# Kernel tuning notes

Hardware: AMD Instinct MI355X
Metric: run time of the kernel (lower is better)

Reference implementation:

```python
import jax, jax.numpy as jnp
import numpy as np

TEMPERATURE = 0.07
BASE_TEMPERATURE = 0.07
EPS = 1e-12


def setup_inputs() -> dict:
    key = jax.random.key(0)
    features = jax.random.normal(key, (4096, 2, 128), dtype=jnp.float32)
    return {"features": features}


def reference(features):
    bsz, n_views, d = features.shape
    n = bsz * n_views
    # torch.cat(torch.unbind(features, dim=1), dim=0): view-major stacking -> [N, D]
    cf = jnp.swapaxes(features, 0, 1).reshape(n, d)
    # L2-normalize rows
    cf = cf / jnp.linalg.norm(cf, axis=-1, keepdims=True)
    # Pairwise L2 distance via Gram matrix: ||a-b||^2 = 2 - 2 a.b for unit vectors.
    # Equivalent math to (cf[:,None]-cf).norm(dim=-1) without the (N,N,D) intermediate.
    gram = cf @ cf.T  # [N, N]
    dist = jnp.sqrt(jnp.clip(2.0 - 2.0 * gram, EPS))
    anchor_dot_contrast = 1.0 - dist  # [N, N]
    logits_max = jax.lax.stop_gradient(jnp.max(anchor_dot_contrast, axis=1, keepdims=True))
    logits = anchor_dot_contrast - logits_max
    # positives mask: same original sample, different row/col in tiled layout
    mask = jnp.tile(jnp.eye(bsz, dtype=jnp.float32), (n_views, n_views))  # [N, N]
    logits_mask = 1.0 - jnp.eye(n, dtype=jnp.float32)  # exclude self
    mask = mask * logits_mask
    exp_logits = jnp.exp(logits) * logits_mask
    log_prob = logits - jnp.log(jnp.sum(exp_logits, axis=1, keepdims=True))
    mean_log_prob_pos = jnp.sum(mask * log_prob, axis=1) / jnp.sum(mask, axis=1)
    loss = -(TEMPERATURE / BASE_TEMPERATURE) * mean_log_prob_pos
    return jnp.mean(loss.reshape(n_views, bsz))
```

## Files before the change

### kernel.cpp

```cpp
#include <hip/hip_runtime.h>
#include <math.h>

#define BSZ   4096
#define NROWS 8192
#define DIM   128
#define EPSC  1e-12f

#define JS  8
#define NJT 8

typedef _Float16 half8 __attribute__((ext_vector_type(8)));
typedef float    f32x4 __attribute__((ext_vector_type(4)));

typedef __attribute__((address_space(1))) const unsigned int gas_u32;
typedef __attribute__((address_space(3))) unsigned int       las_u32;

__device__ __forceinline__ void stageB(_Float16* lds, const char* gsrc, int w, int lane) {
    #pragma unroll
    for (int it = 0; it < 8; ++it) {
        int c = w * 8 + it;
        __builtin_amdgcn_global_load_lds(
            (gas_u32*)(gsrc + c * 1024 + lane * 16),
            (las_u32*)((char*)lds + c * 1024), 16, 0, 0);
    }
}

__global__ __launch_bounds__(256) void norm_zero_kernel(
    const float* __restrict__ feat, float* __restrict__ cf,
    unsigned int* __restrict__ hsw, float* __restrict__ s, float* __restrict__ out)
{
    int t = blockIdx.x * 256 + threadIdx.x;
    if (t < NROWS) s[t] = 0.0f;
    if (t == 0) out[0] = 0.0f;

    int row  = t >> 6;
    int lane = t & 63;
    int v = row >> 12;
    int b = row & 4095;
    const float* src = feat + (size_t)b * 256 + (size_t)v * 128;
    float2 x = *(const float2*)(src + lane * 2);
    float ss = x.x * x.x + x.y * x.y;
    #pragma unroll
    for (int m = 32; m >= 1; m >>= 1) ss += __shfl_xor(ss, m, 64);
    float inv = 1.0f / sqrtf(ss);
    float2 o; o.x = x.x * inv; o.y = x.y * inv;
    *(float2*)(cf + (size_t)row * DIM + lane * 2) = o;

    union { _Float16 h[2]; unsigned int u; } cv;
    cv.h[0] = (_Float16)o.x;
    cv.h[1] = (_Float16)o.y;
    size_t off = (size_t)row * 256 + ((lane * 4) ^ ((row & 7) << 4));
    *(unsigned int*)((char*)hsw + off) = cv.u;
}

__global__ __launch_bounds__(256, 2) void gram_kernel(
    const _Float16* __restrict__ h, float* __restrict__ s)
{
    __shared__ _Float16 bbuf[2][128 * 128];

    int t    = threadIdx.x;
    int w    = t >> 6;
    int lane = t & 63;
    int r16  = lane & 15;
    int g    = lane >> 4;
    int wr   = w >> 1, wc = w & 1;
    int rb   = blockIdx.x >> 3;
    int js   = blockIdx.x & (JS - 1);
    int i0   = rb * 128;
    int rowbase = wr * 64;
    int swz  = (r16 & 7) << 4;
    const char* hb = (const char*)h;

    half8 A[4][4];
    #pragma unroll
    for (int f = 0; f < 4; ++f) {
        size_t rowoff = (size_t)(i0 + rowbase + f * 16 + r16) * 256;
        #pragma unroll
        for (int ks = 0; ks < 4; ++ks)
            A[f][ks] = *(const half8*)(hb + rowoff + ((ks * 64 + g * 16) ^ swz));
    }

    stageB(&bbuf[0][0], hb + (size_t)(js * 1024) * 256, w, lane);

    float rs[4][4];
    #pragma unroll
    for (int a = 0; a < 4; ++a)
        #pragma unroll
        for (int q = 0; q < 4; ++q) rs[a][q] = 0.0f;
    int eq[4];
    #pragma unroll
    for (int q = 0; q < 4; ++q) eq[q] = (g * 4 + q) == r16;

    for (int jt = 0; jt < NJT; ++jt) {
        int j0 = js * 1024 + jt * 128;
        if (jt + 1 < NJT) {
            stageB(&bbuf[(jt + 1) & 1][0], hb + (size_t)(j0 + 128) * 256, w, lane);
            asm volatile("s_waitcnt vmcnt(8)" ::: "memory");
        } else {
            asm volatile("s_waitcnt vmcnt(0)" ::: "memory");
        }
        __builtin_amdgcn_s_barrier();

        const char* bb = (const char*)&bbuf[jt & 1][0];
        f32x4 acc[4][4];
        #pragma unroll
        for (int fr = 0; fr < 4; ++fr)
            #pragma unroll
            for (int fc = 0; fc < 4; ++fc) acc[fr][fc] = (f32x4){0.f, 0.f, 0.f, 0.f};

        #pragma unroll
        for (int ks = 0; ks < 4; ++ks) {
            half8 B[4];
            #pragma unroll
            for (int fc = 0; fc < 4; ++fc)
                B[fc] = *(const half8*)(bb + (wc * 64 + fc * 16 + r16) * 256
                                           + ((ks * 64 + g * 16) ^ swz));
            #pragma unroll
            for (int fr = 0; fr < 4; ++fr)
                #pragma unroll
                for (int fc = 0; fc < 4; ++fc)
                    acc[fr][fc] = __builtin_amdgcn_mfma_f32_16x16x32_f16(
                        A[fr][ks], B[fc], acc[fr][fc], 0, 0, 0);
        }

        int diag_w = (j0 + wc * 64) == (i0 + rowbase);
        #pragma unroll
        for (int fr = 0; fr < 4; ++fr)
            #pragma unroll
            for (int fc = 0; fc < 4; ++fc)
                #pragma unroll
                for (int q = 0; q < 4; ++q) {
                    float gv = acc[fr][fc][q];
                    float t2 = fmaxf(fmaf(-2.0f, gv, 2.0f), EPSC);
                    float e  = __expf(-__builtin_amdgcn_sqrtf(t2));
                    if (diag_w && (fr == fc) && eq[q]) e = 0.0f;
                    rs[fr][q] += e;
                }
        __builtin_amdgcn_s_barrier();
    }

    #pragma unroll
    for (int fr = 0; fr < 4; ++fr)
        #pragma unroll
        for (int q = 0; q < 4; ++q) {
            float v = rs[fr][q];
            v += __shfl_xor(v, 1, 64);
            v += __shfl_xor(v, 2, 64);
            v += __shfl_xor(v, 4, 64);
            v += __shfl_xor(v, 8, 64);
            if (r16 == 0)
                atomicAdd(&s[i0 + rowbase + fr * 16 + g * 4 + q], v);
        }
}

__global__ __launch_bounds__(1024) void finish_kernel(
    const float* __restrict__ cf, const float* __restrict__ s,
    float* __restrict__ out)
{
    __shared__ float red[16];
    int w    = threadIdx.x >> 6;
    int lane = threadIdx.x & 63;
    int i = blockIdx.x * 16 + w;
    int p = (i + BSZ) & (NROWS - 1);
    float2 x = *(const float2*)(cf + (size_t)i * DIM + lane * 2);
    float2 y = *(const float2*)(cf + (size_t)p * DIM + lane * 2);
    float d = x.x * y.x + x.y * y.y;
    #pragma unroll
    for (int m = 32; m >= 1; m >>= 1) d += __shfl_xor(d, m, 64);
    if (lane == 0) {
        float t2  = fmaxf(2.0f - 2.0f * d, EPSC);
        float adc = 1.0f - sqrtf(t2);
        red[w] = 1.0f + logf(s[i]) - adc;
    }
    __syncthreads();
    if (threadIdx.x == 0) {
        float acc = 0.f;
        #pragma unroll
        for (int k = 0; k < 16; ++k) acc += red[k];
        atomicAdd(out, acc * (1.0f / NROWS));
    }
}

extern "C" void kernel_launch(void* const* d_in, const int* in_sizes, int n_in,
                              void* d_out, int out_size, void* d_ws, size_t ws_size,
                              hipStream_t stream)
{
    const float* feat = (const float*)d_in[0];
    float* out = (float*)d_out;
    float* cf  = (float*)d_ws;
    float* s   = cf + (size_t)NROWS * DIM;
    unsigned int* hsw = (unsigned int*)(s + NROWS);

    norm_zero_kernel<<<(NROWS * 64) / 256, 256, 0, stream>>>(feat, cf, hsw, s, out);
    gram_kernel<<<(NROWS / 128) * JS, 256, 0, stream>>>((const _Float16*)hsw, s);
    finish_kernel<<<NROWS / 16, 1024, 0, stream>>>(cf, s, out);
}
```

Baseline: 95.88 us.

## Exploit Gram symmetry: compute upper-triangular tiles with row and column sums

Replaces the full 8192x8192 Gram sweep with one block per upper-triangular 128x128 tile (2080 tiles). Each tile's exp values feed both the row sums and, for off-diagonal tiles, the column sums, which roughly halves the MFMA and transcendental work. In exchange each block does a single tile with no load/compute double-buffering, issues many more atomics (row and column), and needs a sqrt-based mapping from block index to tile.

```diff
diff --git a/kernel.cpp b/kernel.cpp
--- a/kernel.cpp
+++ b/kernel.cpp
@@ -5,9 +5,8 @@
 #define NROWS 8192
 #define DIM   128
 #define EPSC  1e-12f
-
-#define JS  8
-#define NJT 8
+#define NRB   64
+#define NTILES 2080
 
 typedef _Float16 half8 __attribute__((ext_vector_type(8)));
 typedef float    f32x4 __attribute__((ext_vector_type(4)));
@@ -53,10 +52,10 @@
     *(unsigned int*)((char*)hsw + off) = cv.u;
 }
 
-__global__ __launch_bounds__(256, 2) void gram_kernel(
+__global__ __launch_bounds__(256, 2) void gram_tri_kernel(
     const _Float16* __restrict__ h, float* __restrict__ s)
 {
-    __shared__ _Float16 bbuf[2][128 * 128];
+    __shared__ _Float16 bt[128 * 128];
 
     int t    = threadIdx.x;
     int w    = t >> 6;
@@ -64,80 +63,75 @@
     int r16  = lane & 15;
     int g    = lane >> 4;
     int wr   = w >> 1, wc = w & 1;
-    int rb   = blockIdx.x >> 3;
-    int js   = blockIdx.x & (JS - 1);
-    int i0   = rb * 128;
-    int rowbase = wr * 64;
     int swz  = (r16 & 7) << 4;
     const char* hb = (const char*)h;
 
+    int bid = blockIdx.x;
+    int rb = (int)(64.5f - sqrtf(64.5f * 64.5f - 2.0f * (float)bid));
+    rb = rb < 0 ? 0 : (rb > 63 ? 63 : rb);
+    while (rb > 0 && 64 * rb - (rb * (rb - 1)) / 2 > bid) --rb;
+    while (rb < 63 && 64 * (rb + 1) - ((rb + 1) * rb) / 2 <= bid) ++rb;
+    int cb = rb + (bid - (64 * rb - (rb * (rb - 1)) / 2));
+    int i0 = rb * 128, j0 = cb * 128;
+
     half8 A[4][4];
     #pragma unroll
     for (int f = 0; f < 4; ++f) {
-        size_t rowoff = (size_t)(i0 + rowbase + f * 16 + r16) * 256;
+        size_t rowoff = (size_t)(i0 + wr * 64 + f * 16 + r16) * 256;
         #pragma unroll
         for (int ks = 0; ks < 4; ++ks)
             A[f][ks] = *(const half8*)(hb + rowoff + ((ks * 64 + g * 16) ^ swz));
     }
-
-    stageB(&bbuf[0][0], hb + (size_t)(js * 1024) * 256, w, lane);
-
-    float rs[4][4];
-    #pragma unroll
-    for (int a = 0; a < 4; ++a)
-        #pragma unroll
-        for (int q = 0; q < 4; ++q) rs[a][q] = 0.0f;
-    int eq[4];
-    #pragma unroll
-    for (int q = 0; q < 4; ++q) eq[q] = (g * 4 + q) == r16;
-
-    for (int jt = 0; jt < NJT; ++jt) {
-        int j0 = js * 1024 + jt * 128;
-        if (jt + 1 < NJT) {
-            stageB(&bbuf[(jt + 1) & 1][0], hb + (size_t)(j0 + 128) * 256, w, lane);
-            asm volatile("s_waitcnt vmcnt(8)" ::: "memory");
-        } else {
-            asm volatile("s_waitcnt vmcnt(0)" ::: "memory");
-        }
-        __builtin_amdgcn_s_barrier();
-
-        const char* bb = (const char*)&bbuf[jt & 1][0];
-        f32x4 acc[4][4];
-        #pragma unroll
-        for (int fr = 0; fr < 4; ++fr)
-            #pragma unroll
-            for (int fc = 0; fc < 4; ++fc) acc[fr][fc] = (f32x4){0.f, 0.f, 0.f, 0.f};
-
-        #pragma unroll
-        for (int ks = 0; ks < 4; ++ks) {
-            half8 B[4];
-            #pragma unroll
-            for (int fc = 0; fc < 4; ++fc)
-                B[fc] = *(const half8*)(bb + (wc * 64 + fc * 16 + r16) * 256
-                                           + ((ks * 64 + g * 16) ^ swz));
-            #pragma unroll
-            for (int fr = 0; fr < 4; ++fr)
-                #pragma unroll
-                for (int fc = 0; fc < 4; ++fc)
-                    acc[fr][fc] = __builtin_amdgcn_mfma_f32_16x16x32_f16(
-                        A[fr][ks], B[fc], acc[fr][fc], 0, 0, 0);
-        }
-
-        int diag_w = (j0 + wc * 64) == (i0 + rowbase);
+    stageB(bt, hb + (size_t)j0 * 256, w, lane);
+    asm volatile("s_waitcnt vmcnt(0)" ::: "memory");
+    __builtin_amdgcn_s_barrier();
+
+    f32x4 acc[4][4];
+    #pragma unroll
+    for (int fr = 0; fr < 4; ++fr)
+        #pragma unroll
+        for (int fc = 0; fc < 4; ++fc) acc[fr][fc] = (f32x4){0.f, 0.f, 0.f, 0.f};
+
+    const char* bb = (const char*)bt;
+    #pragma unroll
+    for (int ks = 0; ks < 4; ++ks) {
+        half8 B[4];
+        #pragma unroll
+        for (int fc = 0; fc < 4; ++fc)
+            B[fc] = *(const half8*)(bb + (wc * 64 + fc * 16 + r16) * 256
+                                       + ((ks * 64 + g * 16) ^ swz));
         #pragma unroll
         for (int fr = 0; fr < 4; ++fr)
             #pragma unroll
             for (int fc = 0; fc < 4; ++fc)
-                #pragma unroll
-                for (int q = 0; q < 4; ++q) {
-                    float gv = acc[fr][fc][q];
-                    float t2 = fmaxf(fmaf(-2.0f, gv, 2.0f), EPSC);
-                    float e  = __expf(-__builtin_amdgcn_sqrtf(t2));
-                    if (diag_w && (fr == fc) && eq[q]) e = 0.0f;
-                    rs[fr][q] += e;
-                }
-        __builtin_amdgcn_s_barrier();
-    }
+                acc[fr][fc] = __builtin_amdgcn_mfma_f32_16x16x32_f16(
+                    A[fr][ks], B[fc], acc[fr][fc], 0, 0, 0);
+    }
+
+    int dw = (rb == cb) && (wr == wc);
+    int eq[4];
+    #pragma unroll
+    for (int q = 0; q < 4; ++q) eq[q] = (g * 4 + q) == r16;
+
+    float rs[4][4], rc[4] = {0.f, 0.f, 0.f, 0.f};
+    #pragma unroll
+    for (int fr = 0; fr < 4; ++fr)
+        #pragma unroll
+        for (int q = 0; q < 4; ++q) rs[fr][q] = 0.0f;
+
+    #pragma unroll
+    for (int fr = 0; fr < 4; ++fr)
+        #pragma unroll
+        for (int fc = 0; fc < 4; ++fc)
+            #pragma unroll
+            for (int q = 0; q < 4; ++q) {
+                float gv = acc[fr][fc][q];
+                float t2 = fmaxf(fmaf(-2.0f, gv, 2.0f), EPSC);
+                float e  = __expf(-__builtin_amdgcn_sqrtf(t2));
+                if (dw && (fr == fc) && eq[q]) e = 0.0f;
+                rs[fr][q] += e;
+                rc[fc]    += e;
+            }
 
     #pragma unroll
     for (int fr = 0; fr < 4; ++fr)
@@ -149,8 +143,19 @@
             v += __shfl_xor(v, 4, 64);
             v += __shfl_xor(v, 8, 64);
             if (r16 == 0)
-                atomicAdd(&s[i0 + rowbase + fr * 16 + g * 4 + q], v);
+                atomicAdd(&s[i0 + wr * 64 + fr * 16 + g * 4 + q], v);
         }
+
+    if (rb != cb) {
+        #pragma unroll
+        for (int fc = 0; fc < 4; ++fc) {
+            float v = rc[fc];
+            v += __shfl_xor(v, 16, 64);
+            v += __shfl_xor(v, 32, 64);
+            if (g == 0)
+                atomicAdd(&s[j0 + wc * 64 + fc * 16 + r16], v);
+        }
+    }
 }
 
 __global__ __launch_bounds__(1024) void finish_kernel(
@@ -192,6 +197,6 @@
     unsigned int* hsw = (unsigned int*)(s + NROWS);
 
     norm_zero_kernel<<<(NROWS * 64) / 256, 256, 0, stream>>>(feat, cf, hsw, s, out);
-    gram_kernel<<<(NROWS / 128) * JS, 256, 0, stream>>>((const _Float16*)hsw, s);
+    gram_tri_kernel<<<NTILES, 256, 0, stream>>>((const _Float16*)hsw, s);
     finish_kernel<<<NROWS / 16, 1024, 0, stream>>>(cf, s, out);
 }
```

After: 102.0 us. +6.4%, slower.
